# Kernel optimization log

Hardware: AMD Instinct MI355X
Metric: run time of the kernel (lower is better)

Reference implementation:

```python
import jax, jax.numpy as jnp
import numpy as np
import math

EPS = 1e-8
MIN_RADIUS = 0.1
SINH_MAX = math.asinh(2.0 ** 15)
CURV = 1.0                     # exp(clamp(log(1.0), log(0.1), log(10)))
IMAGE_ALPHA = 0.25             # exp(clamp(log(1/4), max=0))
TEXT_ALPHA = 1.0 / 0.6         # exp(log(1/0.6)), frozen
LOGIT_SCALE = 1.0 / 0.07       # exp(clamp(log(1/0.07), max=4.6052))
ENTAIL_WEIGHT = 0.2


def exp_map0(x, curv):
    # MERU exponential map at the Lorentz-model origin (space components only).
    rc = jnp.sqrt(curv) * jnp.linalg.norm(x, axis=-1, keepdims=True)
    sinh_in = jnp.clip(rc, EPS, SINH_MAX)
    return jnp.sinh(sinh_in) * x / jnp.maximum(rc, EPS)


def pairwise_dist(x, y, curv):
    # x: (B,H,W,D) image feats on hyperboloid; y: (C,D) text protos. -> (B,H,W,C)
    x_time = jnp.sqrt(1.0 / curv + jnp.sum(x * x, axis=-1))   # (B,H,W)
    y_time = jnp.sqrt(1.0 / curv + jnp.sum(y * y, axis=-1))   # (C,)
    inner = jnp.einsum('bhwd,cd->bhwc', x, y) - x_time[..., None] * y_time
    c_xyl = -curv * inner
    return jnp.arccosh(jnp.maximum(c_xyl, 1.0 + EPS)) / jnp.sqrt(curv)


def oxy_angle(x, y, curv):
    # Exterior angle at x between origin->x and x->y geodesics. x,y: (...,D) -> (...,)
    x_time = jnp.sqrt(1.0 / curv + jnp.sum(x * x, axis=-1))
    y_time = jnp.sqrt(1.0 / curv + jnp.sum(y * y, axis=-1))
    c_xyl = curv * (jnp.sum(x * y, axis=-1) - x_time * y_time)
    acos_num = y_time + c_xyl * x_time
    acos_den = jnp.linalg.norm(x, axis=-1) * jnp.sqrt(jnp.maximum(c_xyl * c_xyl - 1.0, 0.0))
    acos_in = acos_num / (acos_den + EPS)
    return jnp.arccos(jnp.clip(acos_in, -1.0 + EPS, 1.0 - EPS))


def half_aperture(x, curv):
    asin_in = 2.0 * MIN_RADIUS / (jnp.linalg.norm(x, axis=-1) * jnp.sqrt(curv) + EPS)
    return jnp.arcsin(jnp.clip(asin_in, -1.0 + EPS, 1.0 - EPS))


def _forward(feats, text_protos, labels, mask):
    curv = jnp.float32(CURV)
    img = exp_map0(feats * IMAGE_ALPHA, curv)          # (B,H,W,D)
    txt = exp_map0(text_protos * TEXT_ALPHA, curv)     # (C,D)

    dist = pairwise_dist(img, txt, curv)               # (B,H,W,C)
    proto = txt[labels]                                # (B,H,W,D) gather by GT class
    angle = oxy_angle(proto, img, curv)                # (B,H,W)
    aperture = half_aperture(proto, curv)              # (B,H,W)

    logits = LOGIT_SCALE * (-dist)                     # scale * image_logits
    logp = jax.nn.log_softmax(logits, axis=-1)
    nll = -jnp.take_along_axis(logp, labels[..., None], axis=-1)[..., 0]

    valid = (~mask).astype(jnp.float32)                # mask==1 means ignore
    n_valid = jnp.maximum(jnp.sum(valid), 1.0)
    sup_loss = jnp.sum(nll * valid) / n_valid

    ent = jnp.maximum(angle - aperture, 0.0)
    entail_loss = jnp.sum(ent * valid) / n_valid

    return sup_loss + ENTAIL_WEIGHT * entail_loss


def setup_inputs() -> dict:
    key = jax.random.key(0)
    k1, k2, k3, k4 = jax.random.split(key, 4)
    B, H, W, D, C = 2, 512, 512, 64, 151
    feats = jax.random.normal(k1, (B, H, W, D), dtype=jnp.float32)
    text_protos = jax.random.normal(k2, (C, D), dtype=jnp.float32)
    labels = jax.random.randint(k3, (B, H, W), 0, C, dtype=jnp.int32)
    mask = jax.random.randint(k4, (B, H, W), 0, 2, dtype=jnp.int32).astype(bool)
    return {"feats": feats, "text_protos": text_protos, "labels": labels, "mask": mask}


def reference(feats, text_protos, labels, mask):
    return _forward(feats, text_protos, labels, mask)
```

## Files before the change

### kernel.cpp

```cpp
#include <hip/hip_runtime.h>
#include <math.h>

#define EPSF 1e-8f
#define SINH_MAXF 11.090354888959125f
#define IMAGE_ALPHA 0.25f
#define TEXT_ALPHA (1.0f/0.6f)
#define LOGIT_SCALE (1.0f/0.07f)
#define LN2F 0.6931471805599453f
#define SLN (LOGIT_SCALE*LN2F)
#define ENTAIL_WEIGHT 0.2f
#define NCLS 151
#define NPAD 160
#define DIM 64
#define NBLK 4096

#define LMIN_OFF 8
#define YT_OFF 16
#define XN_OFF (YT_OFF + NPAD)
#define AP_OFF (XN_OFF + NPAD)
#define BT_OFF 512
#define BLK_OFF (BT_OFF + NPAD*DIM/2)

typedef __attribute__((ext_vector_type(8))) short bf16x8;
typedef __attribute__((ext_vector_type(4))) float f32x4;

__device__ inline unsigned short f2bf(float f) {
    unsigned int u = __float_as_uint(f);
    return (unsigned short)((u + 0x7FFFu + ((u >> 16) & 1u)) >> 16);
}
__device__ inline float sel4(const float* a, int i) {
    return i == 0 ? a[0] : i == 1 ? a[1] : i == 2 ? a[2] : a[3];
}
__device__ inline int isel4(const int* a, int i) {
    return i == 0 ? a[0] : i == 1 ? a[1] : i == 2 ? a[2] : a[3];
}

__global__ __launch_bounds__(256) void proto_kernel(const float* __restrict__ protos,
                                                    float* __restrict__ ws) {
    int tid = threadIdx.x, w = tid >> 6, l = tid & 63;
    unsigned short* bt = (unsigned short*)(ws + BT_OFF);
    __shared__ float sYT[NPAD];
    for (int c = w; c < NPAD; c += 4) {
        int t = c >> 4, cn = c & 15;
        int half = l >> 5, g = (l >> 3) & 3, j = l & 7;
        int sidx = (t * 128 + half * 64 + g * 16 + cn) * 8 + j;
        float yt_c;
        if (c < NCLS) {
            float v = protos[c * DIM + l] * TEXT_ALPHA;
            float n2 = v * v;
            #pragma unroll
            for (int m = 32; m >= 1; m >>= 1) n2 += __shfl_xor(n2, m, 64);
            float rc = __builtin_amdgcn_sqrtf(n2);
            float rr = fminf(fmaxf(rc, EPSF), SINH_MAXF);
            float e = __expf(rr);
            float sh = 0.5f * (e - __builtin_amdgcn_rcpf(e));
            float sc = sh * __builtin_amdgcn_rcpf(fmaxf(rc, EPSF));
            bt[sidx] = f2bf(sc * v);
            float xn = sc * rc;
            yt_c = __builtin_amdgcn_sqrtf(fmaf(xn, xn, 1.f));
            if (l == 0) {
                ws[YT_OFF + c] = yt_c;
                ws[XN_OFF + c] = xn;
                float ai = fminf(fmaxf(0.2f / (xn + EPSF), -1.f + EPSF), 1.f - EPSF);
                ws[AP_OFF + c] = asinf(ai);
            }
        } else {
            bt[sidx] = 0;
            yt_c = 2e18f;
            if (l == 0) { ws[YT_OFF + c] = 2e18f; ws[XN_OFF + c] = 1.f; ws[AP_OFF + c] = 0.f; }
        }
        if (l == 0) sYT[c] = yt_c;
    }
    __syncthreads();
    if (tid < 64) {
        float m = 1e30f;
        for (int c = tid; c < NCLS; c += 64) m = fminf(m, sYT[c]);
        #pragma unroll
        for (int k = 32; k >= 1; k >>= 1) m = fminf(m, __shfl_xor(m, k, 64));
        if (tid == 0) ws[LMIN_OFF] = __log2f(2.f * m);
    }
}

struct PixA { bf16x8 q0, q1; float xt, Q; };

__device__ inline PixA stage_pixel(const float4* fp, float lmin2) {
    float4 a0 = fp[0], a1 = fp[1], b0 = fp[8], b1 = fp[9];
    a0.x *= IMAGE_ALPHA; a0.y *= IMAGE_ALPHA; a0.z *= IMAGE_ALPHA; a0.w *= IMAGE_ALPHA;
    a1.x *= IMAGE_ALPHA; a1.y *= IMAGE_ALPHA; a1.z *= IMAGE_ALPHA; a1.w *= IMAGE_ALPHA;
    b0.x *= IMAGE_ALPHA; b0.y *= IMAGE_ALPHA; b0.z *= IMAGE_ALPHA; b0.w *= IMAGE_ALPHA;
    b1.x *= IMAGE_ALPHA; b1.y *= IMAGE_ALPHA; b1.z *= IMAGE_ALPHA; b1.w *= IMAGE_ALPHA;
    float n2 = a0.x*a0.x + a0.y*a0.y + a0.z*a0.z + a0.w*a0.w
             + a1.x*a1.x + a1.y*a1.y + a1.z*a1.z + a1.w*a1.w
             + b0.x*b0.x + b0.y*b0.y + b0.z*b0.z + b0.w*b0.w
             + b1.x*b1.x + b1.y*b1.y + b1.z*b1.z + b1.w*b1.w;
    n2 += __shfl_xor(n2, 16, 64);
    n2 += __shfl_xor(n2, 32, 64);
    float rc = __builtin_amdgcn_sqrtf(n2);
    float rr = fminf(fmaxf(rc, EPSF), SINH_MAXF);
    float e = __expf(rr);
    float sh = 0.5f * (e - __builtin_amdgcn_rcpf(e));
    float sc = sh * __builtin_amdgcn_rcpf(fmaxf(rc, EPSF));
    float xn = sc * rc;
    PixA r;
    r.xt = __builtin_amdgcn_sqrtf(fmaf(xn, xn, 1.f));
    r.Q = SLN * (lmin2 - __log2f(r.xt + xn)) - SLN;
    r.q0[0] = (short)f2bf(sc*a0.x); r.q0[1] = (short)f2bf(sc*a0.y);
    r.q0[2] = (short)f2bf(sc*a0.z); r.q0[3] = (short)f2bf(sc*a0.w);
    r.q0[4] = (short)f2bf(sc*a1.x); r.q0[5] = (short)f2bf(sc*a1.y);
    r.q0[6] = (short)f2bf(sc*a1.z); r.q0[7] = (short)f2bf(sc*a1.w);
    r.q1[0] = (short)f2bf(sc*b0.x); r.q1[1] = (short)f2bf(sc*b0.y);
    r.q1[2] = (short)f2bf(sc*b0.z); r.q1[3] = (short)f2bf(sc*b0.w);
    r.q1[4] = (short)f2bf(sc*b1.x); r.q1[5] = (short)f2bf(sc*b1.y);
    r.q1[6] = (short)f2bf(sc*b1.z); r.q1[7] = (short)f2bf(sc*b1.w);
    return r;
}

__global__ __launch_bounds__(256) void main_kernel(
    const float* __restrict__ feats, const int* __restrict__ labels,
    const unsigned char* __restrict__ mask, const float* __restrict__ wsro,
    float4* __restrict__ blkout)
{
    __shared__ uint4 sBT[1280];
    __shared__ float sYT[NPAD];
    int tid = threadIdx.x;
    const uint4* btg = (const uint4*)(wsro + BT_OFF);
    #pragma unroll
    for (int k = 0; k < 5; k++) sBT[tid + k * 256] = btg[tid + k * 256];
    if (tid < NPAD) sYT[tid] = wsro[YT_OFF + tid];
    __syncthreads();

    int wid = tid >> 6, lane = tid & 63;
    int cn = lane & 15, g = lane >> 4;
    int wavebase = (blockIdx.x * 4 + wid) * 32;
    int pix0 = wavebase + cn, pix1 = pix0 + 16;
    float lmin2 = wsro[LMIN_OFF];

    PixA A0 = stage_pixel((const float4*)(feats + (size_t)pix0 * DIM + g * 8), lmin2);
    PixA A1 = stage_pixel((const float4*)(feats + (size_t)pix1 * DIM + g * 8), lmin2);
    int lab0 = labels[pix0], lab1 = labels[pix1];

    float xtr0[4], Q0[4], xtr1[4], Q1[4];
    int lr0[4], lr1[4];
    #pragma unroll
    for (int r = 0; r < 4; r++) {
        int src = g * 4 + r;
        xtr0[r] = __shfl(A0.xt, src, 64); Q0[r] = __shfl(A0.Q, src, 64);
        lr0[r]  = __shfl(lab0, src, 64);
        xtr1[r] = __shfl(A1.xt, src, 64); Q1[r] = __shfl(A1.Q, src, 64);
        lr1[r]  = __shfl(lab1, src, 64);
    }

    float ss0[4] = {0,0,0,0}, ss1[4] = {0,0,0,0};
    float cx0[4] = {0,0,0,0}, cx1[4] = {0,0,0,0};

    #pragma unroll 2
    for (int t = 0; t < 10; t++) {
        uint4 u0 = sBT[t * 128 + lane];
        uint4 u1 = sBT[t * 128 + 64 + lane];
        bf16x8 bq0 = __builtin_bit_cast(bf16x8, u0);
        bf16x8 bq1 = __builtin_bit_cast(bf16x8, u1);
        float yt = sYT[t * 16 + cn];
        int cls = t * 16 + cn;
        f32x4 d0 = {0,0,0,0}, d1 = {0,0,0,0};
        d0 = __builtin_amdgcn_mfma_f32_16x16x32_bf16(A0.q0, bq0, d0, 0, 0, 0);
        d0 = __builtin_amdgcn_mfma_f32_16x16x32_bf16(A0.q1, bq1, d0, 0, 0, 0);
        d1 = __builtin_amdgcn_mfma_f32_16x16x32_bf16(A1.q0, bq0, d1, 0, 0, 0);
        d1 = __builtin_amdgcn_mfma_f32_16x16x32_bf16(A1.q1, bq1, d1, 0, 0, 0);
        #pragma unroll
        for (int r = 0; r < 4; r++) {
            float c0 = fmaf(xtr0[r], yt, -d0[r]);
            if (lr0[r] == cls) cx0[r] = c0;
            float u0f = __log2f(fmaxf(c0, 1.f + EPSF));
            ss0[r] += __expf(fmaf(-SLN, u0f, Q0[r]));
            float c1 = fmaf(xtr1[r], yt, -d1[r]);
            if (lr1[r] == cls) cx1[r] = c1;
            float u1f = __log2f(fmaxf(c1, 1.f + EPSF));
            ss1[r] += __expf(fmaf(-SLN, u1f, Q1[r]));
        }
    }

    #pragma unroll
    for (int k = 1; k < 16; k <<= 1) {
        #pragma unroll
        for (int r = 0; r < 4; r++) {
            ss0[r] += __shfl_xor(ss0[r], k, 64);
            cx0[r] = fmaxf(cx0[r], __shfl_xor(cx0[r], k, 64));
            ss1[r] += __shfl_xor(ss1[r], k, 64);
            cx1[r] = fmaxf(cx1[r], __shfl_xor(cx1[r], k, 64));
        }
    }

    float v_nll = 0.f, v_ent = 0.f, valid = 0.f;
    if (cn < 4) {
        #pragma unroll
        for (int tile = 0; tile < 2; tile++) {
            float T   = tile ? sel4(ss1, cn) : sel4(ss0, cn);
            float cxl = tile ? sel4(cx1, cn) : sel4(cx0, cn);
            float xts = tile ? sel4(xtr1, cn) : sel4(xtr0, cn);
            float Q   = tile ? sel4(Q1, cn) : sel4(Q0, cn);
            int lb    = tile ? isel4(lr1, cn) : isel4(lr0, cn);
            int pr = wavebase + g * 4 + cn + tile * 16;
            float u = __log2f(fmaxf(cxl, 1.f + EPSF));
            float nll = __logf(T) - Q + SLN * u;
            float pt = wsro[YT_OFF + lb], pn = wsro[XN_OFF + lb], ap = wsro[AP_OFF + lb];
            float num = fmaf(-cxl, pt, xts);
            float den = pn * sqrtf(fmaxf(fmaf(cxl, cxl, -1.f), 0.f));
            float ain = fminf(fmaxf(num / (den + EPSF), -1.f + EPSF), 1.f - EPSF);
            float ent = fmaxf(acosf(ain) - ap, 0.f);
            float vl = mask[pr] ? 0.f : 1.f;
            v_nll += nll * vl; v_ent += ent * vl; valid += vl;
        }
    }

    #pragma unroll
    for (int o = 32; o >= 1; o >>= 1) {
        v_nll += __shfl_down(v_nll, o, 64);
        v_ent += __shfl_down(v_ent, o, 64);
        valid += __shfl_down(valid, o, 64);
    }
    __shared__ float red[3][4];
    if (lane == 0) { red[0][wid] = v_nll; red[1][wid] = v_ent; red[2][wid] = valid; }
    __syncthreads();
    if (tid == 0) {
        float a = 0.f, b = 0.f, c = 0.f;
        #pragma unroll
        for (int w = 0; w < 4; w++) { a += red[0][w]; b += red[1][w]; c += red[2][w]; }
        blkout[blockIdx.x] = make_float4(a, b, c, 0.f);
    }
}

__global__ __launch_bounds__(1024) void reduce_kernel(const float4* __restrict__ blk,
                                                      float* __restrict__ out) {
    float a = 0.f, b = 0.f, c = 0.f;
    for (int i = threadIdx.x; i < NBLK; i += 1024) {
        float4 v = blk[i];
        a += v.x; b += v.y; c += v.z;
    }
    #pragma unroll
    for (int o = 32; o >= 1; o >>= 1) {
        a += __shfl_down(a, o, 64);
        b += __shfl_down(b, o, 64);
        c += __shfl_down(c, o, 64);
    }
    __shared__ float red[3][16];
    int wid = threadIdx.x >> 6, lane = threadIdx.x & 63;
    if (lane == 0) { red[0][wid] = a; red[1][wid] = b; red[2][wid] = c; }
    __syncthreads();
    if (threadIdx.x == 0) {
        float A = 0.f, B = 0.f, C = 0.f;
        #pragma unroll
        for (int w = 0; w < 16; w++) { A += red[0][w]; B += red[1][w]; C += red[2][w]; }
        float n = fmaxf(C, 1.f);
        out[0] = A / n + ENTAIL_WEIGHT * (B / n);
    }
}

extern "C" void kernel_launch(void* const* d_in, const int* in_sizes, int n_in,
                              void* d_out, int out_size, void* d_ws, size_t ws_size,
                              hipStream_t stream) {
    const float* feats  = (const float*)d_in[0];
    const float* protos = (const float*)d_in[1];
    const int* labels   = (const int*)d_in[2];
    const unsigned char* mask = (const unsigned char*)d_in[3];
    float* ws = (float*)d_ws;

    proto_kernel<<<1, 256, 0, stream>>>(protos, ws);

    int npix = in_sizes[2];
    int nblk = npix / 128;
    main_kernel<<<nblk, 256, 0, stream>>>(feats, labels, mask, ws,
                                          (float4*)(ws + BLK_OFF));
    reduce_kernel<<<1, 1024, 0, stream>>>((const float4*)(ws + BLK_OFF), (float*)d_out);
}
```

Baseline: 241.2 us.

## Truncate bf16 packing, drop clamps, gather GT value, approximate acos

Folds the image alpha scale into the per-pixel scalar and packs bf16 pairs by truncation with a byte permute instead of round-to-nearest conversion. The inner loop drops the max-with-one clamp before log2. The ground-truth distance is fetched with a single shuffle from the owning lane instead of a max-reduction across lanes. In the epilogue, acos is replaced by a cubic polynomial approximation, and the divide and sqrt use fast hardware intrinsics. Each change trims ALU work, but truncation, the missing clamp and the polynomial acos all add numerical error.

```diff
diff --git a/kernel.cpp b/kernel.cpp
--- a/kernel.cpp
+++ b/kernel.cpp
@@ -27,6 +27,9 @@
 __device__ inline unsigned short f2bf(float f) {
     unsigned int u = __float_as_uint(f);
     return (unsigned short)((u + 0x7FFFu + ((u >> 16) & 1u)) >> 16);
+}
+__device__ inline unsigned int pack_bf_trunc(float hi, float lo) {
+    return __builtin_amdgcn_perm(__float_as_uint(hi), __float_as_uint(lo), 0x07060302u);
 }
 __device__ inline float sel4(const float* a, int i) {
     return i == 0 ? a[0] : i == 1 ? a[1] : i == 2 ? a[2] : a[3];
@@ -84,34 +87,33 @@
 struct PixA { bf16x8 q0, q1; float xt, Q; };
 
 __device__ inline PixA stage_pixel(const float4* fp, float lmin2) {
-    float4 a0 = fp[0], a1 = fp[1], b0 = fp[8], b1 = fp[9];
-    a0.x *= IMAGE_ALPHA; a0.y *= IMAGE_ALPHA; a0.z *= IMAGE_ALPHA; a0.w *= IMAGE_ALPHA;
-    a1.x *= IMAGE_ALPHA; a1.y *= IMAGE_ALPHA; a1.z *= IMAGE_ALPHA; a1.w *= IMAGE_ALPHA;
-    b0.x *= IMAGE_ALPHA; b0.y *= IMAGE_ALPHA; b0.z *= IMAGE_ALPHA; b0.w *= IMAGE_ALPHA;
-    b1.x *= IMAGE_ALPHA; b1.y *= IMAGE_ALPHA; b1.z *= IMAGE_ALPHA; b1.w *= IMAGE_ALPHA;
-    float n2 = a0.x*a0.x + a0.y*a0.y + a0.z*a0.z + a0.w*a0.w
-             + a1.x*a1.x + a1.y*a1.y + a1.z*a1.z + a1.w*a1.w
-             + b0.x*b0.x + b0.y*b0.y + b0.z*b0.z + b0.w*b0.w
-             + b1.x*b1.x + b1.y*b1.y + b1.z*b1.z + b1.w*b1.w;
-    n2 += __shfl_xor(n2, 16, 64);
-    n2 += __shfl_xor(n2, 32, 64);
-    float rc = __builtin_amdgcn_sqrtf(n2);
+    float4 f0 = fp[0], f1 = fp[1], f2 = fp[8], f3 = fp[9];
+    float n2r = f0.x*f0.x + f0.y*f0.y + f0.z*f0.z + f0.w*f0.w
+              + f1.x*f1.x + f1.y*f1.y + f1.z*f1.z + f1.w*f1.w
+              + f2.x*f2.x + f2.y*f2.y + f2.z*f2.z + f2.w*f2.w
+              + f3.x*f3.x + f3.y*f3.y + f3.z*f3.z + f3.w*f3.w;
+    n2r += __shfl_xor(n2r, 16, 64);
+    n2r += __shfl_xor(n2r, 32, 64);
+    float rc = IMAGE_ALPHA * __builtin_amdgcn_sqrtf(n2r);
     float rr = fminf(fmaxf(rc, EPSF), SINH_MAXF);
     float e = __expf(rr);
     float sh = 0.5f * (e - __builtin_amdgcn_rcpf(e));
     float sc = sh * __builtin_amdgcn_rcpf(fmaxf(rc, EPSF));
     float xn = sc * rc;
+    float k = sc * IMAGE_ALPHA;
     PixA r;
     r.xt = __builtin_amdgcn_sqrtf(fmaf(xn, xn, 1.f));
     r.Q = SLN * (lmin2 - __log2f(r.xt + xn)) - SLN;
-    r.q0[0] = (short)f2bf(sc*a0.x); r.q0[1] = (short)f2bf(sc*a0.y);
-    r.q0[2] = (short)f2bf(sc*a0.z); r.q0[3] = (short)f2bf(sc*a0.w);
-    r.q0[4] = (short)f2bf(sc*a1.x); r.q0[5] = (short)f2bf(sc*a1.y);
-    r.q0[6] = (short)f2bf(sc*a1.z); r.q0[7] = (short)f2bf(sc*a1.w);
-    r.q1[0] = (short)f2bf(sc*b0.x); r.q1[1] = (short)f2bf(sc*b0.y);
-    r.q1[2] = (short)f2bf(sc*b0.z); r.q1[3] = (short)f2bf(sc*b0.w);
-    r.q1[4] = (short)f2bf(sc*b1.x); r.q1[5] = (short)f2bf(sc*b1.y);
-    r.q1[6] = (short)f2bf(sc*b1.z); r.q1[7] = (short)f2bf(sc*b1.w);
+    unsigned int* q0u = (unsigned int*)&r.q0;
+    unsigned int* q1u = (unsigned int*)&r.q1;
+    q0u[0] = pack_bf_trunc(k*f0.y, k*f0.x);
+    q0u[1] = pack_bf_trunc(k*f0.w, k*f0.z);
+    q0u[2] = pack_bf_trunc(k*f1.y, k*f1.x);
+    q0u[3] = pack_bf_trunc(k*f1.w, k*f1.z);
+    q1u[0] = pack_bf_trunc(k*f2.y, k*f2.x);
+    q1u[1] = pack_bf_trunc(k*f2.w, k*f2.z);
+    q1u[2] = pack_bf_trunc(k*f3.y, k*f3.x);
+    q1u[3] = pack_bf_trunc(k*f3.w, k*f3.z);
     return r;
 }
 
@@ -151,7 +153,7 @@
     }
 
     float ss0[4] = {0,0,0,0}, ss1[4] = {0,0,0,0};
-    float cx0[4] = {0,0,0,0}, cx1[4] = {0,0,0,0};
+    float sv0[4] = {0,0,0,0}, sv1[4] = {0,0,0,0};
 
     #pragma unroll 2
     for (int t = 0; t < 10; t++) {
@@ -169,24 +171,27 @@
         #pragma unroll
         for (int r = 0; r < 4; r++) {
             float c0 = fmaf(xtr0[r], yt, -d0[r]);
-            if (lr0[r] == cls) cx0[r] = c0;
-            float u0f = __log2f(fmaxf(c0, 1.f + EPSF));
-            ss0[r] += __expf(fmaf(-SLN, u0f, Q0[r]));
+            if (lr0[r] == cls) sv0[r] = c0;
+            ss0[r] += __expf(fmaf(-SLN, __log2f(c0), Q0[r]));
             float c1 = fmaf(xtr1[r], yt, -d1[r]);
-            if (lr1[r] == cls) cx1[r] = c1;
-            float u1f = __log2f(fmaxf(c1, 1.f + EPSF));
-            ss1[r] += __expf(fmaf(-SLN, u1f, Q1[r]));
-        }
-    }
-
+            if (lr1[r] == cls) sv1[r] = c1;
+            ss1[r] += __expf(fmaf(-SLN, __log2f(c1), Q1[r]));
+        }
+    }
+
+    int gbase = lane & 48;
+    float cx0[4], cx1[4];
+    #pragma unroll
+    for (int r = 0; r < 4; r++) {
+        cx0[r] = __shfl(sv0[r], gbase + (lr0[r] & 15), 64);
+        cx1[r] = __shfl(sv1[r], gbase + (lr1[r] & 15), 64);
+    }
     #pragma unroll
     for (int k = 1; k < 16; k <<= 1) {
         #pragma unroll
         for (int r = 0; r < 4; r++) {
             ss0[r] += __shfl_xor(ss0[r], k, 64);
-            cx0[r] = fmaxf(cx0[r], __shfl_xor(cx0[r], k, 64));
             ss1[r] += __shfl_xor(ss1[r], k, 64);
-            cx1[r] = fmaxf(cx1[r], __shfl_xor(cx1[r], k, 64));
         }
     }
 
@@ -200,13 +205,18 @@
             float Q   = tile ? sel4(Q1, cn) : sel4(Q0, cn);
             int lb    = tile ? isel4(lr1, cn) : isel4(lr0, cn);
             int pr = wavebase + g * 4 + cn + tile * 16;
-            float u = __log2f(fmaxf(cxl, 1.f + EPSF));
-            float nll = __logf(T) - Q + SLN * u;
+            float nll = __logf(T) - Q + SLN * __log2f(cxl);
             float pt = wsro[YT_OFF + lb], pn = wsro[XN_OFF + lb], ap = wsro[AP_OFF + lb];
             float num = fmaf(-cxl, pt, xts);
-            float den = pn * sqrtf(fmaxf(fmaf(cxl, cxl, -1.f), 0.f));
-            float ain = fminf(fmaxf(num / (den + EPSF), -1.f + EPSF), 1.f - EPSF);
-            float ent = fmaxf(acosf(ain) - ap, 0.f);
+            float den = pn * __builtin_amdgcn_sqrtf(fmaxf(fmaf(cxl, cxl, -1.f), 0.f));
+            float ain = num * __builtin_amdgcn_rcpf(den + EPSF);
+            ain = fminf(fmaxf(ain, -1.f + EPSF), 1.f - EPSF);
+            float ax = fabsf(ain);
+            float p = fmaf(fmaf(fmaf(-0.0187293f, ax, 0.0742610f), ax, -0.2121144f),
+                           ax, 1.5707288f);
+            float rr = __builtin_amdgcn_sqrtf(1.f - ax) * p;
+            float ac = ain < 0.f ? 3.14159265358979f - rr : rr;
+            float ent = fmaxf(ac - ap, 0.f);
             float vl = mask[pr] ? 0.f : 1.f;
             v_nll += nll * vl; v_ent += ent * vl; valid += vl;
         }
```

New measurement: 237.9 us. Within noise of the previous version (-1.4%).
